# Kernel optimization log

Hardware: AMD Instinct MI355X
Metric: run time of the kernel (lower is better)

The kernel has to match this reference:

```python
import jax, jax.numpy as jnp
import numpy as np


def setup_inputs() -> dict:
    key = jax.random.key(0)
    k1, k2, k3, k4, k5 = jax.random.split(key, 5)
    B, Ci, Co, H, W, N, K = 8, 256, 256, 128, 128, 4, 3
    x = jax.random.normal(k1, (B, Ci, H, W), dtype=jnp.float32)
    weight = jax.random.normal(k2, (N, Co, Ci, K, K), dtype=jnp.float32)
    styles = jax.random.normal(k3, (B, Ci), dtype=jnp.float32)
    selector = jax.random.uniform(k4, (B, N), dtype=jnp.float32)
    noise = jax.random.normal(k5, (B, Co, H, W), dtype=jnp.float32)
    return {"x": x, "weight": weight, "styles": styles,
            "selector": selector, "noise": noise}


def reference(x, weight, styles, selector, noise):
    """Modulated conv2d with adaptive kernel selection (fused_modconv path).

    x:        [B, Ci, H, W]
    weight:   [N, Co, Ci, kh, kw]  kernel bank
    styles:   [B, Ci]              modulation
    selector: [B, N]               adaptive kernel mixing coefficients
    noise:    [B, Co, H, W]        additive noise
    """
    B, Ci, H, W = x.shape
    N, Co, _, kh, kw = weight.shape

    # adaptive kernel selection: per-sample kernel = selector-weighted sum of bank
    w = jnp.einsum('bn,noihw->boihw', selector, weight)          # [B,Co,Ci,kh,kw]

    # modulate by styles
    w = w * styles[:, None, :, None, None]

    # demodulate
    dcoefs = jax.lax.rsqrt(jnp.sum(w * w, axis=(2, 3, 4)) + 1e-8)  # [B,Co]
    w = w * dcoefs[:, :, None, None, None]

    # fused per-sample conv via grouped conv (groups = B), cross-correlation
    # (flip_weight=True in the torch code means plain conv2d / cross-correlation)
    xr = x.reshape(1, B * Ci, H, W)
    wr = w.reshape(B * Co, Ci, kh, kw)
    out = jax.lax.conv_general_dilated(
        xr, wr,
        window_strides=(1, 1),
        padding=[(kh // 2, kh // 2), (kw // 2, kw // 2)],
        feature_group_count=B,
        dimension_numbers=('NCHW', 'OIHW', 'NCHW'),
    )
    out = out.reshape(B, Co, H, W) + noise
    return out
```

## Files before the change

### kernel.cpp

```cpp
#include <hip/hip_runtime.h>


typedef __attribute__((ext_vector_type(4))) float f32x4;
typedef __attribute__((ext_vector_type(8))) short s16x8;

#define NB   8
#define NCI  256
#define NCO  256
#define NHW  128
#define NKER 4

#define SB0 __builtin_amdgcn_sched_barrier(0)
#define BAR __builtin_amdgcn_s_barrier()
#define WAITV(N) asm volatile("s_waitcnt vmcnt(" #N ")" ::: "memory")
#define WAITL0   asm volatile("s_waitcnt lgkmcnt(0)" ::: "memory")

__device__ __forceinline__ unsigned short f2bf(float f) {
  unsigned int u = __builtin_bit_cast(unsigned int, f);
  u += 0x7FFFu + ((u >> 16) & 1u);
  return (unsigned short)(u >> 16);
}

__device__ __forceinline__ void gl_lds16(const void* g, void* l) {
  __builtin_amdgcn_global_load_lds(
      (const __attribute__((address_space(1))) void*)(unsigned long long)(uintptr_t)g,
      (__attribute__((address_space(3))) void*)(unsigned int)(uintptr_t)l,
      16, 0, 0);
}

__global__ __launch_bounds__(256) void prep_k(
    const float* __restrict__ weight,
    const float* __restrict__ styles,
    const float* __restrict__ selector,
    unsigned short* __restrict__ wmod)
{
  int bid = blockIdx.x;
  int b = bid >> 8, co = bid & 255;
  int ci = threadIdx.x;

  float sel[NKER];
#pragma unroll
  for (int n = 0; n < NKER; ++n) sel[n] = selector[b * NKER + n];

  float a[9];
#pragma unroll
  for (int j = 0; j < 9; ++j) a[j] = 0.f;
#pragma unroll
  for (int n = 0; n < NKER; ++n) {
    const float* wp = weight + (size_t)((n * NCO + co) * NCI + ci) * 9;
    float s = sel[n];
#pragma unroll
    for (int j = 0; j < 9; ++j) a[j] += s * wp[j];
  }
  float st = styles[b * NCI + ci];
  float ss = 0.f;
#pragma unroll
  for (int j = 0; j < 9; ++j) { a[j] *= st; ss += a[j] * a[j]; }

  for (int off = 32; off; off >>= 1) ss += __shfl_down(ss, off, 64);
  __shared__ float red[4];
  int wid = threadIdx.x >> 6, lane = threadIdx.x & 63;
  if (lane == 0) red[wid] = ss;
  __syncthreads();
  float tot = red[0] + red[1] + red[2] + red[3];
  float d = rsqrtf(tot + 1e-8f);

  int kb = ci >> 5, ci5 = ci & 31;
  int row = co >> 1;
  int slot = (((co & 1) << 2) + (ci5 >> 3)) ^ (row & 7);
  int boff = (slot << 4) + ((ci5 & 7) << 1);
#pragma unroll
  for (int j = 0; j < 9; ++j) {
    size_t T = (size_t)((b * 9 + j) * 8 + kb);
    wmod[(T << 13) + (row << 6) + (boff >> 1)] = f2bf(a[j] * d);
  }
}

__global__ __launch_bounds__(256, 2) void conv_k(
    const float* __restrict__ x,
    const unsigned short* __restrict__ wg,
    const float* __restrict__ noise,
    float* __restrict__ out)
{
  extern __shared__ __align__(16) char smem[];
  char* AlB = smem;
  char* XRs = smem + 3 * 16384;

  int orig = blockIdx.x;
  int b = orig & 7;
  int h = orig >> 3;

  int t = threadIdx.x;
  int lane = t & 63;
  int wid = t >> 6;
  int cow = wid << 6;
  int ll = lane & 15;
  int ks = lane >> 4;

  f32x4 acc[4][8];
#pragma unroll
  for (int m = 0; m < 4; ++m)
#pragma unroll
    for (int n = 0; n < 8; ++n) acc[m][n] = (f32x4){0.f, 0.f, 0.f, 0.f};

  int c = ((t >> 4) & 15) * 2;
  int wi = t & 15;
  float xlo[8], xhi[8];
  unsigned xmask = 0xFFFFFFFFu;

  auto issueX = [&](int g) {
    int gc = g < 24 ? g : 23;
    int dh = gc >> 3, kb = gc & 7;
    int hy = h + dh - 1;
    xmask = ((unsigned)hy < 128u) ? 0xFFFFFFFFu : 0u;
    int hyc = hy < 0 ? 0 : (hy > 127 ? 127 : hy);
    const float* base = x + ((size_t)(b * NCI + kb * 32 + c) * NHW + hyc) * NHW + wi;
#pragma unroll
    for (int j2 = 0; j2 < 8; ++j2) {
      xlo[j2] = base[j2 * 16];
      xhi[j2] = base[NHW * NHW + j2 * 16];
    }
  };

  auto issueA = [&](int tc, char* dst) {
    if (tc > 71) tc = 71;
    int g = tc / 3, tap = tc - g * 3;
    int dh = g >> 3, kb = g & 7;
    const char* src = (const char*)wg +
        ((size_t)((b * 9 + dh * 3 + tap) * 8 + kb) << 14);
#pragma unroll
    for (int i = 0; i < 4; ++i) {
      int ch = wid * 4 + i;
      gl_lds16(src + ch * 1024 + lane * 16, dst + ch * 1024 + lane * 16);
    }
  };

  auto packXR = [&](int g) {
    char* dstb = XRs + (g & 1) * 8192;
    int slot = (((wi & 1) << 2) + (c >> 3)) ^ ((wi >> 1) & 7);
    char* p0 = dstb + (wi >> 1) * 128 + (slot << 4) + ((c & 7) << 1);
#pragma unroll
    for (int j2 = 0; j2 < 8; ++j2) {
      unsigned pk = ((unsigned)f2bf(xhi[j2]) << 16) | f2bf(xlo[j2]);
      *(unsigned*)(p0 + j2 * 1024) = pk & xmask;
    }
  };

  auto readAF = [&](const char* Ab, s16x8* af) {
#pragma unroll
    for (int m = 0; m < 4; ++m) {
      int co = cow + m * 16 + ll;
      int row = co >> 1;
      int slot = (((co & 1) << 2) + ks) ^ (row & 7);
      af[m] = *(const s16x8*)(Ab + row * 128 + (slot << 4));
    }
  };

#define PFB(XRBASE, DW, bf)                                              \
  {                                                                      \
    const char* Xb = (XRBASE);                                           \
    _Pragma("unroll")                                                    \
    for (int n = 0; n < 8; ++n) {                                        \
      int wn = n * 16 + ll + (DW) - 1;                                   \
      if (((DW) == 0 && n == 0) || ((DW) == 2 && n == 7)) {              \
        int wx = wn < 0 ? 0 : (wn > 127 ? 127 : wn);                     \
        int row = wx >> 1;                                               \
        int slot = (((wx & 1) << 2) + ks) ^ (row & 7);                   \
        s16x8 bv = *(const s16x8*)(Xb + row * 128 + (slot << 4));        \
        if (wn != wx) { s16x8 z = {0, 0, 0, 0, 0, 0, 0, 0}; bv = z; }    \
        bf[n] = bv;                                                      \
      } else {                                                           \
        int row = wn >> 1;                                               \
        int slot = (((wn & 1) << 2) + ks) ^ (row & 7);                   \
        bf[n] = *(const s16x8*)(Xb + row * 128 + (slot << 4));           \
      }                                                                  \
    }                                                                    \
  }

#define MFMA32(af, bf)                                                   \
  __builtin_amdgcn_s_setprio(1);                                         \
  _Pragma("unroll")                                                      \
  for (int m = 0; m < 4; ++m)                                            \
    _Pragma("unroll")                                                    \
    for (int n = 0; n < 8; ++n)                                          \
      acc[m][n] = __builtin_amdgcn_mfma_f32_16x16x32_bf16(               \
          af[m], bf[n], acc[m][n], 0, 0, 0);                             \
  __builtin_amdgcn_s_setprio(0);

  s16x8 bfA[8], bfB[8], af[4];

  issueX(0); SB0;
  issueA(0, AlB); SB0;
  issueA(1, AlB + 16384); SB0;
  WAITV(8); SB0;
  packXR(0);
  WAITV(4); SB0;
  WAITL0; SB0;
  BAR; SB0;
  PFB(XRs, 0, bfA);

#pragma unroll 1
  for (int gg = 0; gg < 12; ++gg) {
    int t0 = gg * 6;
    int g0 = gg * 2;
    WAITV(4); SB0; BAR; SB0;
    issueA(t0 + 2, AlB + 2 * 16384); SB0;
    issueX(g0 + 1); SB0;
    readAF(AlB, af);
    PFB(XRs, 1, bfB);
    MFMA32(af, bfA);
    WAITV(20); SB0; BAR; SB0;
    issueA(t0 + 3, AlB); SB0;
    WAITV(4); SB0;
    packXR(g0 + 1);
    readAF(AlB + 16384, af);
    PFB(XRs, 2, bfA);
    MFMA32(af, bfB);
    WAITL0; SB0;
    WAITV(4); SB0; BAR; SB0;
    issueA(t0 + 4, AlB + 16384); SB0;
    readAF(AlB + 2 * 16384, af);
    PFB(XRs + 8192, 0, bfB);
    MFMA32(af, bfA);
    WAITV(4); SB0; BAR; SB0;
    issueA(t0 + 5, AlB + 2 * 16384); SB0;
    issueX(g0 + 2); SB0;
    readAF(AlB, af);
    PFB(XRs + 8192, 1, bfA);
    MFMA32(af, bfB);
    WAITV(20); SB0; BAR; SB0;
    issueA(t0 + 6, AlB); SB0;
    WAITV(4); SB0;
    packXR(g0 + 2);
    readAF(AlB + 16384, af);
    PFB(XRs + 8192, 2, bfB);
    MFMA32(af, bfA);
    WAITL0; SB0;
    WAITV(4); SB0; BAR; SB0;
    issueA(t0 + 7, AlB + 16384); SB0;
    readAF(AlB + 2 * 16384, af);
    PFB(XRs, 0, bfA);
    MFMA32(af, bfB);
  }

  int pr4 = ks * 4;
#pragma unroll
  for (int m = 0; m < 4; ++m) {
#pragma unroll
    for (int n = 0; n < 8; ++n) {
      int px = n * 16 + ll;
#pragma unroll
      for (int j = 0; j < 4; ++j) {
        int co = cow + m * 16 + pr4 + j;
        size_t idx = ((size_t)(b * NCO + co) * NHW + h) * NHW + px;
        out[idx] = acc[m][n][j] + noise[idx];
      }
    }
  }
}

extern "C" void kernel_launch(void* const* d_in, const int* in_sizes, int n_in,
                              void* d_out, int out_size, void* d_ws, size_t ws_size,
                              hipStream_t stream) {
  const float* x        = (const float*)d_in[0];
  const float* weight   = (const float*)d_in[1];
  const float* styles   = (const float*)d_in[2];
  const float* selector = (const float*)d_in[3];
  const float* noise    = (const float*)d_in[4];
  float* out = (float*)d_out;

  unsigned short* wmod = (unsigned short*)d_ws;

  hipLaunchKernelGGL(prep_k, dim3(NB * NCO), dim3(256), 0, stream,
                     weight, styles, selector, wmod);
  hipLaunchKernelGGL(conv_k, dim3(NB * NHW), dim3(256), 64 * 1024, stream,
                     x, wmod, noise, out);
}
```

Baseline: 204.8 us.

## Load weight fragments directly from global into registers, bypassing LDS

The prep kernel now writes the modulated weights in an MFMA-fragment order, so each lane can read its A operand straight from global memory into registers. The triple-buffered LDS staging of weights and its vmcnt waits are removed, which cuts LDS use from 64KB to 16KB per block. This could allow more resident blocks and removes the LDS round trip for weights. The cost is that global-load latency now sits directly in front of the MFMAs. Each wave also reads weights from L2 separately, and the B fragment is reloaded serially with less double buffering.

New measurement: 174.5 us (median of 2 runs). 1.17x faster.

```diff
diff --git a/kernel.cpp b/kernel.cpp
--- a/kernel.cpp
+++ b/kernel.cpp
@@ -12,20 +12,12 @@
 
 #define SB0 __builtin_amdgcn_sched_barrier(0)
 #define BAR __builtin_amdgcn_s_barrier()
-#define WAITV(N) asm volatile("s_waitcnt vmcnt(" #N ")" ::: "memory")
-#define WAITL0   asm volatile("s_waitcnt lgkmcnt(0)" ::: "memory")
+#define WAITL0 asm volatile("s_waitcnt lgkmcnt(0)" ::: "memory")
 
 __device__ __forceinline__ unsigned short f2bf(float f) {
   unsigned int u = __builtin_bit_cast(unsigned int, f);
   u += 0x7FFFu + ((u >> 16) & 1u);
   return (unsigned short)(u >> 16);
-}
-
-__device__ __forceinline__ void gl_lds16(const void* g, void* l) {
-  __builtin_amdgcn_global_load_lds(
-      (const __attribute__((address_space(1))) void*)(unsigned long long)(uintptr_t)g,
-      (__attribute__((address_space(3))) void*)(unsigned int)(uintptr_t)l,
-      16, 0, 0);
 }
 
 __global__ __launch_bounds__(256) void prep_k(
@@ -65,14 +57,13 @@
   float tot = red[0] + red[1] + red[2] + red[3];
   float d = rsqrtf(tot + 1e-8f);
 
-  int kb = ci >> 5, ci5 = ci & 31;
-  int row = co >> 1;
-  int slot = (((co & 1) << 2) + (ci5 >> 3)) ^ (row & 7);
-  int boff = (slot << 4) + ((ci5 & 7) << 1);
+  int kb = ci >> 5;
+  size_t base = (size_t)(co >> 4) * 512 +
+                (size_t)(((ci & 31) >> 3) * 128) + ((co & 15) * 8) + (ci & 7);
 #pragma unroll
   for (int j = 0; j < 9; ++j) {
     size_t T = (size_t)((b * 9 + j) * 8 + kb);
-    wmod[(T << 13) + (row << 6) + (boff >> 1)] = f2bf(a[j] * d);
+    wmod[(T << 13) + base] = f2bf(a[j] * d);
   }
 }
 
@@ -82,9 +73,7 @@
     const float* __restrict__ noise,
     float* __restrict__ out)
 {
-  extern __shared__ __align__(16) char smem[];
-  char* AlB = smem;
-  char* XRs = smem + 3 * 16384;
+  extern __shared__ __align__(16) char XRs[];
 
   int orig = blockIdx.x;
   int b = orig & 7;
@@ -122,17 +111,15 @@
     }
   };
 
-  auto issueA = [&](int tc, char* dst) {
+  auto issueAF = [&](int tc, s16x8* af) {
     if (tc > 71) tc = 71;
     int g = tc / 3, tap = tc - g * 3;
     int dh = g >> 3, kb = g & 7;
     const char* src = (const char*)wg +
-        ((size_t)((b * 9 + dh * 3 + tap) * 8 + kb) << 14);
-#pragma unroll
-    for (int i = 0; i < 4; ++i) {
-      int ch = wid * 4 + i;
-      gl_lds16(src + ch * 1024 + lane * 16, dst + ch * 1024 + lane * 16);
-    }
+        ((size_t)((b * 9 + dh * 3 + tap) * 8 + kb) << 14) + wid * 4096 + lane * 16;
+#pragma unroll
+    for (int m = 0; m < 4; ++m)
+      af[m] = *(const s16x8*)(src + m * 1024);
   };
 
   auto packXR = [&](int g) {
@@ -143,16 +130,6 @@
     for (int j2 = 0; j2 < 8; ++j2) {
       unsigned pk = ((unsigned)f2bf(xhi[j2]) << 16) | f2bf(xlo[j2]);
       *(unsigned*)(p0 + j2 * 1024) = pk & xmask;
-    }
-  };
-
-  auto readAF = [&](const char* Ab, s16x8* af) {
-#pragma unroll
-    for (int m = 0; m < 4; ++m) {
-      int co = cow + m * 16 + ll;
-      int row = co >> 1;
-      int slot = (((co & 1) << 2) + ks) ^ (row & 7);
-      af[m] = *(const s16x8*)(Ab + row * 128 + (slot << 4));
     }
   };
 
@@ -187,60 +164,39 @@
           af[m], bf[n], acc[m][n], 0, 0, 0);                             \
   __builtin_amdgcn_s_setprio(0);
 
-  s16x8 bfA[8], bfB[8], af[4];
+  s16x8 afA[4], afB[4], bf[8];
 
   issueX(0); SB0;
-  issueA(0, AlB); SB0;
-  issueA(1, AlB + 16384); SB0;
-  WAITV(8); SB0;
+  issueAF(0, afA); SB0;
   packXR(0);
-  WAITV(4); SB0;
-  WAITL0; SB0;
-  BAR; SB0;
-  PFB(XRs, 0, bfA);
 
 #pragma unroll 1
   for (int gg = 0; gg < 12; ++gg) {
-    int t0 = gg * 6;
-    int g0 = gg * 2;
-    WAITV(4); SB0; BAR; SB0;
-    issueA(t0 + 2, AlB + 2 * 16384); SB0;
+    int g0 = gg * 2, t0 = gg * 6;
+    WAITL0; SB0; BAR; SB0;
+    PFB(XRs, 0, bf);
+    issueAF(t0 + 1, afB); SB0;
     issueX(g0 + 1); SB0;
-    readAF(AlB, af);
-    PFB(XRs, 1, bfB);
-    MFMA32(af, bfA);
-    WAITV(20); SB0; BAR; SB0;
-    issueA(t0 + 3, AlB); SB0;
-    WAITV(4); SB0;
+    MFMA32(afA, bf);
+    PFB(XRs, 1, bf);
+    issueAF(t0 + 2, afA); SB0;
+    MFMA32(afB, bf);
+    PFB(XRs, 2, bf);
+    issueAF(t0 + 3, afB); SB0;
     packXR(g0 + 1);
-    readAF(AlB + 16384, af);
-    PFB(XRs, 2, bfA);
-    MFMA32(af, bfB);
-    WAITL0; SB0;
-    WAITV(4); SB0; BAR; SB0;
-    issueA(t0 + 4, AlB + 16384); SB0;
-    readAF(AlB + 2 * 16384, af);
-    PFB(XRs + 8192, 0, bfB);
-    MFMA32(af, bfA);
-    WAITV(4); SB0; BAR; SB0;
-    issueA(t0 + 5, AlB + 2 * 16384); SB0;
+    MFMA32(afA, bf);
+    WAITL0; SB0; BAR; SB0;
+    PFB(XRs + 8192, 0, bf);
+    issueAF(t0 + 4, afA); SB0;
     issueX(g0 + 2); SB0;
-    readAF(AlB, af);
-    PFB(XRs + 8192, 1, bfA);
-    MFMA32(af, bfB);
-    WAITV(20); SB0; BAR; SB0;
-    issueA(t0 + 6, AlB); SB0;
-    WAITV(4); SB0;
+    MFMA32(afB, bf);
+    PFB(XRs + 8192, 1, bf);
+    issueAF(t0 + 5, afB); SB0;
+    MFMA32(afA, bf);
+    PFB(XRs + 8192, 2, bf);
+    issueAF(t0 + 6, afA); SB0;
     packXR(g0 + 2);
-    readAF(AlB + 16384, af);
-    PFB(XRs + 8192, 2, bfB);
-    MFMA32(af, bfA);
-    WAITL0; SB0;
-    WAITV(4); SB0; BAR; SB0;
-    issueA(t0 + 7, AlB + 16384); SB0;
-    readAF(AlB + 2 * 16384, af);
-    PFB(XRs, 0, bfA);
-    MFMA32(af, bfB);
+    MFMA32(afB, bf);
   }
 
   int pr4 = ks * 4;
@@ -273,6 +229,6 @@
 
   hipLaunchKernelGGL(prep_k, dim3(NB * NCO), dim3(256), 0, stream,
                      weight, styles, selector, wmod);
-  hipLaunchKernelGGL(conv_k, dim3(NB * NHW), dim3(256), 64 * 1024, stream,
+  hipLaunchKernelGGL(conv_k, dim3(NB * NHW), dim3(256), 16 * 1024, stream,
                      x, wmod, noise, out);
 }
```
